# Kernel tuning notes

Hardware: AMD Instinct MI355X
Metric: run time of the kernel (lower is better)

## Reference

```python
import jax, jax.numpy as jnp
import numpy as np

OFFSET = 3  # windows 3,5,7


def _maxpool_same(x, k):
    # MaxPool2d(kernel=k, stride=1, padding=(k-1)//2); torch pads with -inf
    p = (k - 1) // 2
    return jax.lax.reduce_window(
        x, -jnp.inf, jax.lax.max,
        window_dimensions=(1, 1, k, k),
        window_strides=(1, 1, 1, 1),
        padding=((0, 0), (0, 0), (p, p), (p, p)))


def setup_inputs() -> dict:
    key = jax.random.key(0)
    # strictly positive so log10 is finite
    x = jax.random.uniform(key, (8, 64, 256, 256), dtype=jnp.float32,
                           minval=1e-3, maxval=1.0)
    return {"x": x}


def reference(x) -> jnp.ndarray:
    B, C, H, W = x.shape
    windows = jnp.array([2.0 * i + 1.0 for i in range(1, OFFSET + 1)],
                        dtype=x.dtype)  # [3,5,7]
    xs = jnp.log10(windows / (H * W))
    xc = xs - xs.mean()
    # Closed-form OLS slope weights: inv(X X^T) X reduces analytically to
    # w_i = (x_i - xbar) / sum_j (x_j - xbar)^2 for the slope row.
    w = xc / jnp.sum(xc * xc)                  # [OFFSET]
    # slope = sum_i w_i * log10(maxpool_{k_i}(x)), computed without stacking
    holder = jnp.zeros_like(x)
    for i in range(OFFSET):
        k = 2 * (i + 1) + 1
        holder = holder + w[i] * jnp.log10(_maxpool_same(x, k))
    return holder  # (B, C, H, W)
```

## Files before the change

kernel.cpp:

```cpp
#include <hip/hip_runtime.h>
#include <cmath>


#define IMG_H 256
#define IMG_W 256
#define RPW   8
#define NR    14
#define WPB   4

typedef float vf4 __attribute__((ext_vector_type(4)));

__device__ __forceinline__ vf4 aload(const float* base, uint32_t voff) {
  vf4 r;
  asm volatile("global_load_dwordx4 %0, %1, %2"
               : "=v"(r) : "v"(voff), "s"(base) : "memory");
  return r;
}

__device__ __forceinline__ void wait_first10(vf4& a, vf4& b, vf4& c, vf4& d,
                                             vf4& e, vf4& f, vf4& g, vf4& h,
                                             vf4& i, vf4& j) {
  asm volatile("s_waitcnt vmcnt(4)"
               : "+v"(a), "+v"(b), "+v"(c), "+v"(d), "+v"(e),
                 "+v"(f), "+v"(g), "+v"(h), "+v"(i), "+v"(j) :: "memory");
}

__device__ __forceinline__ void wait_last4(vf4& a, vf4& b, vf4& c, vf4& d) {
  asm volatile("s_waitcnt vmcnt(4)"
               : "+v"(a), "+v"(b), "+v"(c), "+v"(d) :: "memory");
}

__device__ __forceinline__ float dpp_left(float v) {
  return __int_as_float(
      __builtin_amdgcn_update_dpp(0, __float_as_int(v), 0x138, 0xF, 0xF, true));
}
__device__ __forceinline__ float dpp_right(float v) {
  return __int_as_float(
      __builtin_amdgcn_update_dpp(0, __float_as_int(v), 0x130, 0xF, 0xF, true));
}

__device__ __forceinline__ vf4 vmax(vf4 a, vf4 b) {
  vf4 r;
  r.x = fmaxf(a.x, b.x); r.y = fmaxf(a.y, b.y);
  r.z = fmaxf(a.z, b.z); r.w = fmaxf(a.w, b.w);
  return r;
}

struct PS { float p1, p2, p3, s1, s2, s3, f; };

__device__ __forceinline__ PS make_ps(vf4 a) {
  PS r;
  r.p1 = a.x;
  r.p2 = fmaxf(a.x, a.y);
  r.p3 = fmaxf(r.p2, a.z);
  r.s1 = a.w;
  r.s2 = fmaxf(a.z, a.w);
  r.s3 = fmaxf(a.y, r.s2);
  r.f  = fmaxf(r.p2, r.s2);
  return r;
}

__device__ __forceinline__ vf4 row_out(vf4 wm3, vf4 wm2, vf4 wm1, vf4 wc,
                                       vf4 wp1, vf4 wp2, vf4 wp3,
                                       float w3, float w5, float w7) {
  vf4 v1 = vmax(vmax(wm1, wc), wp1);
  vf4 v2 = vmax(v1, vmax(wm2, wp2));
  vf4 v3 = vmax(v2, vmax(wm3, wp3));

  PS a1 = make_ps(v1), a2 = make_ps(v2), a3 = make_ps(v3);

  float L1s1 = dpp_left(a1.s1);
  float L2s1 = dpp_left(a2.s1);
  float L2s2 = dpp_left(a2.s2);
  float L3s1 = dpp_left(a3.s1);
  float L3s2 = dpp_left(a3.s2);
  float L3s3 = dpp_left(a3.s3);

  float R1p1 = dpp_right(a1.p1);
  float R2p1 = dpp_right(a2.p1);
  float R2p2 = dpp_right(a2.p2);
  float R3p1 = dpp_right(a3.p1);
  float R3p2 = dpp_right(a3.p2);
  float R3p3 = dpp_right(a3.p3);

  float m3_0 = fmaxf(L1s1, a1.p2);
  float m3_1 = a1.p3;
  float m3_2 = a1.s3;
  float m3_3 = fmaxf(a1.s2, R1p1);

  float m5_0 = fmaxf(L2s2, a2.p3);
  float m5_1 = fmaxf(L2s1, a2.f);
  float m5_2 = fmaxf(a2.f, R2p1);
  float m5_3 = fmaxf(a2.s3, R2p2);

  float m7_0 = fmaxf(L3s3, a3.f);
  float m7_1 = fmaxf(fmaxf(L3s2, a3.f), R3p1);
  float m7_2 = fmaxf(fmaxf(L3s1, a3.f), R3p2);
  float m7_3 = fmaxf(a3.f, R3p3);

  vf4 o;
  o.x = fmaf(w7, __log2f(m7_0), fmaf(w5, __log2f(m5_0), w3 * __log2f(m3_0)));
  o.y = fmaf(w7, __log2f(m7_1), fmaf(w5, __log2f(m5_1), w3 * __log2f(m3_1)));
  o.z = fmaf(w7, __log2f(m7_2), fmaf(w5, __log2f(m5_2), w3 * __log2f(m3_2)));
  o.w = fmaf(w7, __log2f(m7_3), fmaf(w5, __log2f(m5_3), w3 * __log2f(m3_3)));
  return o;
}

__global__ __launch_bounds__(256, 6) void holder_kernel(
    const float* __restrict__ x, float* __restrict__ out,
    float w3, float w5, float w7)
{
  const int lane = threadIdx.x & 63;
  const int wave = threadIdx.x >> 6;
  const int img  = blockIdx.y;
  const int r0   = blockIdx.x * (WPB * RPW) + wave * RPW;

  const float* px = x + (size_t)img * (IMG_H * IMG_W);
  float*       po = out + (size_t)img * (IMG_H * IMG_W) + lane * 4;
  const uint32_t lo = (uint32_t)lane * 16u;

  const vf4 vzero = (vf4)0.0f;

  vf4 w[NR];
#pragma unroll
  for (int i = 0; i < NR; ++i) {
    int rr = r0 - 3 + i;
    int rc = rr < 0 ? 0 : (rr > IMG_H - 1 ? IMG_H - 1 : rr);
    w[i] = aload(px, (uint32_t)(rc * IMG_W * 4) + lo);
  }

  wait_first10(w[0], w[1], w[2], w[3], w[4], w[5], w[6], w[7], w[8], w[9]);
#pragma unroll
  for (int i = 0; i < 10; ++i) {
    if (r0 - 3 + i < 0) w[i] = vzero;
  }

#pragma unroll
  for (int j = 0; j < 4; ++j) {
    vf4 o = row_out(w[j], w[j + 1], w[j + 2], w[j + 3],
                    w[j + 4], w[j + 5], w[j + 6], w3, w5, w7);
    *(vf4*)(po + (r0 + j) * IMG_W) = o;
  }

  wait_last4(w[10], w[11], w[12], w[13]);
#pragma unroll
  for (int i = 10; i < NR; ++i) {
    if (r0 - 3 + i >= IMG_H) w[i] = vzero;
  }

#pragma unroll
  for (int j = 4; j < 8; ++j) {
    vf4 o = row_out(w[j], w[j + 1], w[j + 2], w[j + 3],
                    w[j + 4], w[j + 5], w[j + 6], w3, w5, w7);
    *(vf4*)(po + (r0 + j) * IMG_W) = o;
  }
}

extern "C" void kernel_launch(void* const* d_in, const int* in_sizes, int n_in,
                              void* d_out, int out_size, void* d_ws, size_t ws_size,
                              hipStream_t stream) {
  const float* x = (const float*)d_in[0];
  float* out = (float*)d_out;

  const int n_img = in_sizes[0] / (IMG_H * IMG_W);

  const double l0 = log10(3.0), l1 = log10(5.0), l2 = log10(7.0);
  const double m  = (l0 + l1 + l2) / 3.0;
  const double c0 = l0 - m, c1 = l1 - m, c2 = l2 - m;
  const double s  = c0 * c0 + c1 * c1 + c2 * c2;
  const double LG2 = 0.30102999566398119521;
  const float w3 = (float)(c0 / s * LG2);
  const float w5 = (float)(c1 / s * LG2);
  const float w7 = (float)(c2 / s * LG2);

  hipLaunchKernelGGL(holder_kernel, dim3(IMG_H / (WPB * RPW), n_img), dim3(256),
                     0, stream, x, out, w3, w5, w7);
}
```

Measured before the change: 229.6 us.

## Stage block row tile plus halo in LDS to cut redundant global loads

```diff
diff --git a/kernel.cpp b/kernel.cpp
--- a/kernel.cpp
+++ b/kernel.cpp
@@ -5,8 +5,9 @@
 #define IMG_H 256
 #define IMG_W 256
 #define RPW   8
-#define NR    14
 #define WPB   4
+#define BROWS (WPB * RPW)
+#define LROWS (BROWS + 6)
 
 typedef float vf4 __attribute__((ext_vector_type(4)));
 
@@ -17,17 +18,12 @@
   return r;
 }
 
-__device__ __forceinline__ void wait_first10(vf4& a, vf4& b, vf4& c, vf4& d,
-                                             vf4& e, vf4& f, vf4& g, vf4& h,
-                                             vf4& i, vf4& j) {
-  asm volatile("s_waitcnt vmcnt(4)"
+__device__ __forceinline__ void wait0_10(vf4& a, vf4& b, vf4& c, vf4& d,
+                                         vf4& e, vf4& f, vf4& g, vf4& h,
+                                         vf4& i, vf4& j) {
+  asm volatile("s_waitcnt vmcnt(0)"
                : "+v"(a), "+v"(b), "+v"(c), "+v"(d), "+v"(e),
                  "+v"(f), "+v"(g), "+v"(h), "+v"(i), "+v"(j) :: "memory");
-}
-
-__device__ __forceinline__ void wait_last4(vf4& a, vf4& b, vf4& c, vf4& d) {
-  asm volatile("s_waitcnt vmcnt(4)"
-               : "+v"(a), "+v"(b), "+v"(c), "+v"(d) :: "memory");
 }
 
 __device__ __forceinline__ float dpp_left(float v) {
@@ -106,14 +102,14 @@
   return o;
 }
 
-__global__ __launch_bounds__(256, 6) void holder_kernel(
+__global__ __launch_bounds__(256, 4) void holder_kernel(
     const float* __restrict__ x, float* __restrict__ out,
     float w3, float w5, float w7)
 {
   const int lane = threadIdx.x & 63;
   const int wave = threadIdx.x >> 6;
   const int img  = blockIdx.y;
-  const int r0   = blockIdx.x * (WPB * RPW) + wave * RPW;
+  const int r0   = blockIdx.x * BROWS;
 
   const float* px = x + (size_t)img * (IMG_H * IMG_W);
   float*       po = out + (size_t)img * (IMG_H * IMG_W) + lane * 4;
@@ -121,38 +117,41 @@
 
   const vf4 vzero = (vf4)0.0f;
 
-  vf4 w[NR];
+  __shared__ float lds[LROWS][IMG_W];
+
+  vf4 st[10];
 #pragma unroll
-  for (int i = 0; i < NR; ++i) {
-    int rr = r0 - 3 + i;
+  for (int k = 0; k < 10; ++k) {
+    int lrow = wave + k * WPB;
+    if (lrow > LROWS - 1) lrow = LROWS - 1;
+    int rr = r0 - 3 + lrow;
     int rc = rr < 0 ? 0 : (rr > IMG_H - 1 ? IMG_H - 1 : rr);
-    w[i] = aload(px, (uint32_t)(rc * IMG_W * 4) + lo);
+    st[k] = aload(px, (uint32_t)(rc * IMG_W * 4) + lo);
   }
-
-  wait_first10(w[0], w[1], w[2], w[3], w[4], w[5], w[6], w[7], w[8], w[9]);
+  wait0_10(st[0], st[1], st[2], st[3], st[4],
+           st[5], st[6], st[7], st[8], st[9]);
 #pragma unroll
-  for (int i = 0; i < 10; ++i) {
-    if (r0 - 3 + i < 0) w[i] = vzero;
+  for (int k = 0; k < 10; ++k) {
+    int lrow = wave + k * WPB;
+    if (lrow > LROWS - 1) lrow = LROWS - 1;
+    int rr = r0 - 3 + lrow;
+    vf4 v = (rr < 0 || rr >= IMG_H) ? vzero : st[k];
+    *(vf4*)&lds[lrow][lane * 4] = v;
   }
+  __syncthreads();
 
 #pragma unroll
-  for (int j = 0; j < 4; ++j) {
-    vf4 o = row_out(w[j], w[j + 1], w[j + 2], w[j + 3],
-                    w[j + 4], w[j + 5], w[j + 6], w3, w5, w7);
-    *(vf4*)(po + (r0 + j) * IMG_W) = o;
-  }
-
-  wait_last4(w[10], w[11], w[12], w[13]);
-#pragma unroll
-  for (int i = 10; i < NR; ++i) {
-    if (r0 - 3 + i >= IMG_H) w[i] = vzero;
-  }
-
-#pragma unroll
-  for (int j = 4; j < 8; ++j) {
-    vf4 o = row_out(w[j], w[j + 1], w[j + 2], w[j + 3],
-                    w[j + 4], w[j + 5], w[j + 6], w3, w5, w7);
-    *(vf4*)(po + (r0 + j) * IMG_W) = o;
+  for (int j = 0; j < RPW; ++j) {
+    const int lb = wave * RPW + j;
+    vf4 o = row_out(*(const vf4*)&lds[lb + 0][lane * 4],
+                    *(const vf4*)&lds[lb + 1][lane * 4],
+                    *(const vf4*)&lds[lb + 2][lane * 4],
+                    *(const vf4*)&lds[lb + 3][lane * 4],
+                    *(const vf4*)&lds[lb + 4][lane * 4],
+                    *(const vf4*)&lds[lb + 5][lane * 4],
+                    *(const vf4*)&lds[lb + 6][lane * 4],
+                    w3, w5, w7);
+    *(vf4*)(po + (r0 + wave * RPW + j) * IMG_W) = o;
   }
 }
 
@@ -173,6 +172,6 @@
   const float w5 = (float)(c1 / s * LG2);
   const float w7 = (float)(c2 / s * LG2);
 
-  hipLaunchKernelGGL(holder_kernel, dim3(IMG_H / (WPB * RPW), n_img), dim3(256),
+  hipLaunchKernelGGL(holder_kernel, dim3(IMG_H / BROWS, n_img), dim3(256),
                      0, stream, x, out, w3, w5, w7);
 }
```

Measured after the change: 229.0 us. Within noise of the previous version (-0.2%).

## Stream 64-row strips per wave with a register ring buffer and prefetch

Applied to the files above, without the earlier changes.

```diff
diff --git a/kernel.cpp b/kernel.cpp
--- a/kernel.cpp
+++ b/kernel.cpp
@@ -4,9 +4,8 @@
 
 #define IMG_H 256
 #define IMG_W 256
-#define RPW   8
-#define NR    14
-#define WPB   4
+#define SROWS 64
+#define LEAD  8
 
 typedef float vf4 __attribute__((ext_vector_type(4)));
 
@@ -17,17 +16,19 @@
   return r;
 }
 
-__device__ __forceinline__ void wait_first10(vf4& a, vf4& b, vf4& c, vf4& d,
-                                             vf4& e, vf4& f, vf4& g, vf4& h,
-                                             vf4& i, vf4& j) {
-  asm volatile("s_waitcnt vmcnt(4)"
-               : "+v"(a), "+v"(b), "+v"(c), "+v"(d), "+v"(e),
-                 "+v"(f), "+v"(g), "+v"(h), "+v"(i), "+v"(j) :: "memory");
+__device__ __forceinline__ void wait_all11(vf4& a, vf4& b, vf4& c, vf4& d,
+                                           vf4& e, vf4& f, vf4& g, vf4& h,
+                                           vf4& i, vf4& j, vf4& k) {
+  asm volatile("s_waitcnt vmcnt(0)"
+               : "+v"(a), "+v"(b), "+v"(c), "+v"(d), "+v"(e), "+v"(f),
+                 "+v"(g), "+v"(h), "+v"(i), "+v"(j), "+v"(k) :: "memory");
 }
 
-__device__ __forceinline__ void wait_last4(vf4& a, vf4& b, vf4& c, vf4& d) {
-  asm volatile("s_waitcnt vmcnt(4)"
-               : "+v"(a), "+v"(b), "+v"(c), "+v"(d) :: "memory");
+__device__ __forceinline__ void wait10_w7(vf4& a, vf4& b, vf4& c, vf4& d,
+                                          vf4& e, vf4& f, vf4& g) {
+  asm volatile("s_waitcnt vmcnt(10)"
+               : "+v"(a), "+v"(b), "+v"(c), "+v"(d), "+v"(e), "+v"(f),
+                 "+v"(g) :: "memory");
 }
 
 __device__ __forceinline__ float dpp_left(float v) {
@@ -106,14 +107,14 @@
   return o;
 }
 
-__global__ __launch_bounds__(256, 6) void holder_kernel(
+__global__ __launch_bounds__(64, 2) void holder_kernel(
     const float* __restrict__ x, float* __restrict__ out,
     float w3, float w5, float w7)
 {
-  const int lane = threadIdx.x & 63;
-  const int wave = threadIdx.x >> 6;
-  const int img  = blockIdx.y;
-  const int r0   = blockIdx.x * (WPB * RPW) + wave * RPW;
+  const int lane  = threadIdx.x;
+  const int img   = blockIdx.x;
+  const int strip = blockIdx.y;
+  const int r0    = strip * SROWS;
 
   const float* px = x + (size_t)img * (IMG_H * IMG_W);
   float*       po = out + (size_t)img * (IMG_H * IMG_W) + lane * 4;
@@ -121,38 +122,38 @@
 
   const vf4 vzero = (vf4)0.0f;
 
-  vf4 w[NR];
-#pragma unroll
-  for (int i = 0; i < NR; ++i) {
-    int rr = r0 - 3 + i;
-    int rc = rr < 0 ? 0 : (rr > IMG_H - 1 ? IMG_H - 1 : rr);
-    w[i] = aload(px, (uint32_t)(rc * IMG_W * 4) + lo);
-  }
-
-  wait_first10(w[0], w[1], w[2], w[3], w[4], w[5], w[6], w[7], w[8], w[9]);
-#pragma unroll
-  for (int i = 0; i < 10; ++i) {
-    if (r0 - 3 + i < 0) w[i] = vzero;
-  }
+  vf4 ring[16];
 
 #pragma unroll
-  for (int j = 0; j < 4; ++j) {
-    vf4 o = row_out(w[j], w[j + 1], w[j + 2], w[j + 3],
-                    w[j + 4], w[j + 5], w[j + 6], w3, w5, w7);
-    *(vf4*)(po + (r0 + j) * IMG_W) = o;
+  for (int i = 0; i < 11; ++i) {
+    int rr = r0 - 3 + i;
+    int rc = rr < 0 ? 0 : rr;
+    ring[(i + 13) & 15] = aload(px, (uint32_t)(rc * IMG_W * 4) + lo);
   }
+  wait_all11(ring[13], ring[14], ring[15], ring[0], ring[1], ring[2],
+             ring[3], ring[4], ring[5], ring[6], ring[7]);
+  if (r0 == 0) { ring[13] = vzero; ring[14] = vzero; ring[15] = vzero; }
 
-  wait_last4(w[10], w[11], w[12], w[13]);
+#pragma unroll 1
+  for (int it = 0; it < SROWS / 16; ++it) {
+    const int R = r0 + it * 16;
 #pragma unroll
-  for (int i = 10; i < NR; ++i) {
-    if (r0 - 3 + i >= IMG_H) w[i] = vzero;
-  }
-
-#pragma unroll
-  for (int j = 4; j < 8; ++j) {
-    vf4 o = row_out(w[j], w[j + 1], w[j + 2], w[j + 3],
-                    w[j + 4], w[j + 5], w[j + 6], w3, w5, w7);
-    *(vf4*)(po + (r0 + j) * IMG_W) = o;
+    for (int k = 0; k < 16; ++k) {
+      {
+        int rr = R + k + LEAD;
+        int rc = rr > IMG_H - 1 ? IMG_H - 1 : rr;
+        ring[(k + LEAD) & 15] = aload(px, (uint32_t)(rc * IMG_W * 4) + lo);
+      }
+      wait10_w7(ring[(k + 13) & 15], ring[(k + 14) & 15], ring[(k + 15) & 15],
+                ring[k & 15], ring[(k + 1) & 15], ring[(k + 2) & 15],
+                ring[(k + 3) & 15]);
+      if (R + k + 3 > IMG_H - 1) ring[(k + 3) & 15] = vzero;
+      vf4 o = row_out(ring[(k + 13) & 15], ring[(k + 14) & 15],
+                      ring[(k + 15) & 15], ring[k & 15],
+                      ring[(k + 1) & 15], ring[(k + 2) & 15],
+                      ring[(k + 3) & 15], w3, w5, w7);
+      *(vf4*)(po + (R + k) * IMG_W) = o;
+    }
   }
 }
 
@@ -173,6 +174,6 @@
   const float w5 = (float)(c1 / s * LG2);
   const float w7 = (float)(c2 / s * LG2);
 
-  hipLaunchKernelGGL(holder_kernel, dim3(IMG_H / (WPB * RPW), n_img), dim3(256),
+  hipLaunchKernelGGL(holder_kernel, dim3(n_img, IMG_H / SROWS), dim3(64),
                      0, stream, x, out, w3, w5, w7);
 }
```

New measurement: 235.4 us. 2.5% more time.
